# Kernel tuning notes

Measured on AMD Instinct MI355X. Metric: run time of the kernel, lower is better.

## Reference

```python
import jax, jax.numpy as jnp
import numpy as np

N, C, H, W = 32, 2, 512, 512


def setup_inputs() -> dict:
    key = jax.random.key(0)
    k1, k2, k3, k4 = jax.random.split(key, 4)
    inputs = jax.random.uniform(k1, (N, C, H, W), dtype=jnp.float32)
    targets = jax.random.randint(k2, (N, H, W), 0, C, dtype=jnp.int64)
    classes_weights = jax.random.uniform(k3, (C,), dtype=jnp.float32)
    tiles_weights = jax.random.uniform(k4, (N,), dtype=jnp.float32)
    return {"inputs": inputs, "targets": targets,
            "classes_weights": classes_weights, "tiles_weights": tiles_weights,
            "config": 0}


def reference(inputs, targets, classes_weights, tiles_weights, config):
    n, c, h, w = inputs.shape
    p = h * w
    # [C, N, P] layout: vectorize the original's nested class/sample loops
    x = jnp.transpose(inputs.reshape(n, c, p), (1, 0, 2))
    masks = (targets.reshape(n, p)[None] == jnp.arange(c)[:, None, None]).astype(inputs.dtype)
    distance = jnp.abs(masks - x)
    order = jnp.argsort(-distance, axis=-1)  # descending sort per (class, sample)
    d_sorted = jnp.take_along_axis(distance, order, axis=-1)
    m_sorted = jnp.take_along_axis(masks, order, axis=-1)
    gts = jnp.sum(m_sorted, axis=-1, keepdims=True)
    inter = gts - jnp.cumsum(m_sorted, axis=-1)
    union = gts + jnp.cumsum(1.0 - m_sorted, axis=-1)
    iou = 1.0 - inter / union
    # Lovasz gradient: first element kept, then first differences
    grad = jnp.concatenate([iou[..., :1], iou[..., 1:] - iou[..., :-1]], axis=-1)
    per = jnp.sum(d_sorted * grad, axis=-1)  # [C, N]
    # skip condition from original: empty mask AND no prediction above 0.25
    empty = (jnp.sum(masks, axis=-1) == 0) & (jnp.sum(x > 0.25, axis=-1) == 0)
    valid = (classes_weights != 0.0)[:, None] & (~empty)
    weighted = per * tiles_weights[None, :] * classes_weights[:, None]
    loss = jnp.sum(jnp.where(valid, weighted, 0.0))
    non_empty = jnp.sum(valid).astype(inputs.dtype)
    return loss / n / non_empty
```

## Files before the change

kernel.cpp:

```cpp
#include <hip/hip_runtime.h>
#include <hip/hip_bf16.h>
#include <hip/hip_cooperative_groups.h>


#define NB    2048
#define NSEG  64
#define PLOG  18
#define NN    32
#define PTOT  (1 << PLOG)
#define CHUNK (NB / 256)
#define B0_LO (NB / 4)
#define B1_HI (3 * NB / 4)

namespace cg = cooperative_groups;


__device__ __forceinline__ void hist_body(
    const float* __restrict__ x, const int* __restrict__ tgt,
    unsigned* __restrict__ partial, int Bn, int g, unsigned* hl)
{
    const int n = g / Bn, sl = g - n * Bn;
    const int tid = threadIdx.x;
    for (int i = tid; i < 2 * NB; i += 256) hl[i] = 0;
    __syncthreads();

    const int pairs = PTOT / Bn;
    const int base  = sl * pairs;
    const float* x0 = x + (((long long)n * 2) << PLOG);
    const float* x1 = x0 + PTOT;
    const int*   tg = tgt + ((long long)n << PLOG);

    for (int off = tid * 4; off < pairs; off += 256 * 4) {
        const int p = base + off;
        float4 a  = *(const float4*)(x0 + p);
        float4 b  = *(const float4*)(x1 + p);
        int4   t4 = *(const int4*)(tg + p);
        float xa[4] = {a.x, a.y, a.z, a.w};
        float xb[4] = {b.x, b.y, b.z, b.w};
        int   tt[4] = {t4.x, t4.y, t4.z, t4.w};
#pragma unroll
        for (int k = 0; k < 4; ++k) {
            const bool m0 = (tt[k] == 0);
            const bool m1 = (tt[k] == 1);
            float d0 = m0 ? 1.0f - xa[k] : xa[k];
            float d1 = m1 ? 1.0f - xb[k] : xb[k];
            int b0 = min((int)(d0 * (float)NB), NB - 1);
            int b1 = min((int)(d1 * (float)NB), NB - 1);
            atomicAdd(&hl[b0],      m0 ? 0x10000u : 1u);
            atomicAdd(&hl[NB + b1], m1 ? 0x10000u : 1u);
        }
    }
    __syncthreads();
    unsigned* outp = partial + (size_t)g * (2 * NB);
    for (int i = tid; i < 2 * NB; i += 256) outp[i] = hl[i];
}

__device__ __forceinline__ void merge_body(unsigned* __restrict__ partial,
                                           int Bn, int mb)
{
    const int parts = NB / 256;
    const int seg  = mb / parts;
    const int part = mb - seg * parts;
    const int c = seg >> 5, n = seg & 31;
    const int b = part * 256 + threadIdx.x;

    unsigned v0 = 0, v1 = 0;
    for (int s = 0; s < Bn; ++s) {
        unsigned v = partial[(((size_t)(n * Bn + s) * 2) + c) * NB + b];
        v0 += v & 0xFFFFu; v1 += v >> 16;
    }
    partial[(((size_t)(n * Bn + 0) * 2) + c) * NB + b] = v0;
    partial[(((size_t)(n * Bn + 1) * 2) + c) * NB + b] = v1;
}

__device__ __forceinline__ void scan_body(
    const unsigned* __restrict__ partial,
    const float* __restrict__ cw, const float* __restrict__ tw,
    float* __restrict__ segval, unsigned* __restrict__ segvalid,
    int Bn, int seg, unsigned* mh, unsigned* red)
{
    const int c = seg >> 5, n = seg & 31;
    const int tid = threadIdx.x;

    const unsigned* p0 = partial + (((size_t)(n * Bn + 0) * 2) + c) * NB;
    const unsigned* p1 = partial + (((size_t)(n * Bn + 1) * 2) + c) * NB;
    for (int i = tid; i < NB; i += 256) { mh[i] = p0[i]; mh[NB + i] = p1[i]; }
    __syncthreads();

    unsigned tot_all = 0, tot1 = 0, cgt = 0;
    int maxb_local = -1;
    for (int j = 0; j < CHUNK; ++j) {
        int b = (NB - 1) - (tid * CHUNK + j);
        unsigned n0 = mh[b], n1 = mh[NB + b];
        tot_all += n0 + n1; tot1 += n1;
        if (b >= B0_LO) cgt += n0;
        if (b <  B1_HI) cgt += n1;
        if (maxb_local < 0 && (n0 | n1)) maxb_local = b;
    }
    unsigned* sa = red;
    unsigned* s1 = red + 256;
    unsigned* sc = red + 512;
    sa[tid] = tot_all; s1[tid] = tot1; sc[tid] = cgt;
    __syncthreads();
    for (int off = 1; off < 256; off <<= 1) {
        unsigned va = 0, v1 = 0, vc = 0;
        if (tid >= off) { va = sa[tid - off]; v1 = s1[tid - off]; vc = sc[tid - off]; }
        __syncthreads();
        sa[tid] += va; s1[tid] += v1; sc[tid] += vc;
        __syncthreads();
    }
    const unsigned gts   = s1[255];
    const unsigned cntgt = sc[255];
    const unsigned i0  = (tid > 0) ? sa[tid - 1] : 0;
    const unsigned sc0 = (tid > 0) ? s1[tid - 1] : 0;
    __syncthreads();
    ((int*)sc)[tid] = maxb_local;
    __syncthreads();
    for (int off = 128; off > 0; off >>= 1) {
        if (tid < off) ((int*)sc)[tid] = max(((int*)sc)[tid], ((int*)sc)[tid + off]);
        __syncthreads();
    }
    const int max_b = ((int*)sc)[0];

    float per_local = 0.0f;
    if (gts > 0) {
        unsigned i = i0, s = sc0;
        for (int j = 0; j < CHUNK; ++j) {
            int b = (NB - 1) - (tid * CHUNK + j);
            unsigned n0 = mh[b], n1 = mh[NB + b];
            if (n0 | n1) {
                float d_rep = ((float)b + 0.5f) * (1.0f / (float)NB);
                float U = (float)(gts + i - s);
                if (n1) per_local += (float)n1 * d_rep / U;
                s += n1;
                unsigned inter = gts - s;
                if (n0 && inter)
                    per_local += d_rep * (float)inter * (float)n0 /
                                 (U * (U + (float)n0));
                i += n0 + n1;
            }
        }
    }
    __syncthreads();
    float* sd = (float*)sa;
    sd[tid] = per_local;
    __syncthreads();
    for (int off = 128; off > 0; off >>= 1) {
        if (tid < off) sd[tid] += sd[tid + off];
        __syncthreads();
    }
    if (tid == 0) {
        float per = sd[0];
        if (gts == 0)
            per = (max_b >= 0) ? ((float)max_b + 0.5f) * (1.0f / (float)NB) : 0.0f;
        const bool empty = (gts == 0) && (cntgt == 0);
        const float cwv = cw[c], twv = tw[n];
        const bool valid = (cwv != 0.0f) && !empty;
        segval[seg]   = valid ? per * twv * cwv : 0.0f;
        segvalid[seg] = valid ? 1u : 0u;
    }
}

__device__ __forceinline__ void final_body(const float* __restrict__ segval,
                                           const unsigned* __restrict__ segvalid,
                                           float* __restrict__ out)
{
    const int tid = threadIdx.x;
    if (tid < 64) {
        float    lv = segval[tid];
        unsigned vv = segvalid[tid];
        for (int off = 32; off > 0; off >>= 1) {
            lv += __shfl_down(lv, off);
            vv += __shfl_down(vv, off);
        }
        if (tid == 0) out[0] = lv / (float)NN / (float)vv;
    }
}

__global__ __launch_bounds__(256, 8) void lovasz_fused_kernel(
    const float* __restrict__ x, const int* __restrict__ tgt,
    unsigned* __restrict__ partial, float* __restrict__ segval,
    unsigned* __restrict__ segvalid, const float* __restrict__ cw,
    const float* __restrict__ tw, float* __restrict__ out)
{
    __shared__ unsigned hl[2 * NB];
    __shared__ unsigned red[768];
    cg::grid_group grid = cg::this_grid();

    hist_body(x, tgt, partial, 64, blockIdx.x, hl);
    grid.sync();
    if (blockIdx.x < NSEG * (NB / 256))
        merge_body(partial, 64, blockIdx.x);
    grid.sync();
    if (blockIdx.x < NSEG)
        scan_body(partial, cw, tw, segval, segvalid, 64, blockIdx.x, hl, red);
    grid.sync();
    if (blockIdx.x == 0)
        final_body(segval, segvalid, out);
}

__global__ __launch_bounds__(256, 8) void hist_k(
    const float* __restrict__ x, const int* __restrict__ tgt,
    unsigned* __restrict__ partial, int Bn)
{
    __shared__ unsigned hl[2 * NB];
    hist_body(x, tgt, partial, Bn, blockIdx.x, hl);
}

__global__ __launch_bounds__(256) void merge_k(unsigned* __restrict__ partial, int Bn)
{
    merge_body(partial, Bn, blockIdx.x);
}

__global__ __launch_bounds__(256) void scan_k(
    const unsigned* __restrict__ partial, const float* __restrict__ cw,
    const float* __restrict__ tw, float* __restrict__ segval,
    unsigned* __restrict__ segvalid, int Bn)
{
    __shared__ unsigned mh[2 * NB];
    __shared__ unsigned red[768];
    scan_body(partial, cw, tw, segval, segvalid, Bn, blockIdx.x, mh, red);
}

__global__ void final_k(const float* __restrict__ segval,
                        const unsigned* __restrict__ segvalid,
                        float* __restrict__ out)
{
    final_body(segval, segvalid, out);
}

extern "C" void kernel_launch(void* const* d_in, const int* in_sizes, int n_in,
                              void* d_out, int out_size, void* d_ws, size_t ws_size,
                              hipStream_t stream)
{
    const float* x   = (const float*)d_in[0];
    const int*   tgt = (const int*)d_in[1];
    const float* cw  = (const float*)d_in[2];
    const float* tw  = (const float*)d_in[3];
    float* out = (float*)d_out;

    float*    segval   = (float*)d_ws;
    unsigned* segvalid = (unsigned*)((char*)d_ws + 256);
    unsigned* partial  = (unsigned*)((char*)d_ws + 512);

    const size_t per_bn = (size_t)NN * 2 * NB * sizeof(unsigned);
    int Bn = 0;
    if      (ws_size >= 512 + 64 * per_bn) Bn = 64;
    else if (ws_size >= 512 + 32 * per_bn) Bn = 32;
    else                                   Bn = 16;

    bool coop = false;
    if (Bn == 64) {
        int occ = 0, ncu = 0;
        if (hipOccupancyMaxActiveBlocksPerMultiprocessor(
                &occ, lovasz_fused_kernel, 256, 0) == hipSuccess) {
            hipDeviceProp_t prop;
            int dev = 0;
            hipGetDevice(&dev);
            if (hipGetDeviceProperties(&prop, dev) == hipSuccess)
                ncu = prop.multiProcessorCount;
            coop = ((long long)occ * ncu >= (long long)NN * 64);
        }
    }

    if (coop) {
        void* args[] = {(void*)&x, (void*)&tgt, (void*)&partial, (void*)&segval,
                        (void*)&segvalid, (void*)&cw, (void*)&tw, (void*)&out};
        hipLaunchCooperativeKernel((void*)lovasz_fused_kernel,
                                   dim3(NN * 64), dim3(256), args, 0, stream);
    } else {
        hist_k <<<NN * Bn, 256, 0, stream>>>(x, tgt, partial, Bn);
        merge_k<<<NSEG * (NB / 256), 256, 0, stream>>>(partial, Bn);
        scan_k <<<NSEG, 256, 0, stream>>>(partial, cw, tw, segval, segvalid, Bn);
        final_k<<<1, 64, 0, stream>>>(segval, segvalid, out);
    }
}
```

Before: 150.0 us.

## Replace cooperative grid-sync kernel with two launches and atomic final reduction

Drops the cooperative fused kernel and its three grid-wide barriers. The work now runs as two ordinary launches: a histogram kernel, then a merge+scan kernel with 1024-thread blocks that sums partial histograms straight into shared memory. The final reduction moves into the scan kernel through atomics and a last-block-done counter. This removes grid syncs and the separate merge and final passes, but the merge now runs on only 64 blocks, each reading 64 partial histograms, which may underuse the GPU.

```diff
diff --git a/kernel.cpp b/kernel.cpp
--- a/kernel.cpp
+++ b/kernel.cpp
@@ -1,6 +1,5 @@
 #include <hip/hip_runtime.h>
 #include <hip/hip_bf16.h>
-#include <hip/hip_cooperative_groups.h>
 
 
 #define NB    2048
@@ -8,19 +7,27 @@
 #define PLOG  18
 #define NN    32
 #define PTOT  (1 << PLOG)
-#define CHUNK (NB / 256)
 #define B0_LO (NB / 4)
 #define B1_HI (3 * NB / 4)
-
-namespace cg = cooperative_groups;
+#define ST    1024
+#define SCH   (NB / ST)
 
 
-__device__ __forceinline__ void hist_body(
+__global__ __launch_bounds__(256, 8) void hist_k(
     const float* __restrict__ x, const int* __restrict__ tgt,
-    unsigned* __restrict__ partial, int Bn, int g, unsigned* hl)
+    unsigned* __restrict__ partial, float* __restrict__ loss_sum,
+    unsigned* __restrict__ valid_cnt, unsigned* __restrict__ done, int Bn)
 {
-    const int n = g / Bn, sl = g - n * Bn;
+    __shared__ unsigned hl[2 * NB];
+    const int g   = blockIdx.x;
+    const int n   = g / Bn;
+    const int sl  = g - n * Bn;
     const int tid = threadIdx.x;
+
+    if (g == 0 && tid == 0) {
+        *loss_sum = 0.0f; *valid_cnt = 0u; *done = 0u;
+    }
+
     for (int i = tid; i < 2 * NB; i += 256) hl[i] = 0;
     __syncthreads();
 
@@ -55,68 +62,56 @@
     for (int i = tid; i < 2 * NB; i += 256) outp[i] = hl[i];
 }
 
-__device__ __forceinline__ void merge_body(unsigned* __restrict__ partial,
-                                           int Bn, int mb)
+__global__ __launch_bounds__(ST) void mergescan_k(
+    const unsigned* __restrict__ partial, const float* __restrict__ cw,
+    const float* __restrict__ tw, float* __restrict__ loss_sum,
+    unsigned* __restrict__ valid_cnt, unsigned* __restrict__ done,
+    float* __restrict__ out, int Bn)
 {
-    const int parts = NB / 256;
-    const int seg  = mb / parts;
-    const int part = mb - seg * parts;
-    const int c = seg >> 5, n = seg & 31;
-    const int b = part * 256 + threadIdx.x;
-
-    unsigned v0 = 0, v1 = 0;
-    for (int s = 0; s < Bn; ++s) {
-        unsigned v = partial[(((size_t)(n * Bn + s) * 2) + c) * NB + b];
-        v0 += v & 0xFFFFu; v1 += v >> 16;
-    }
-    partial[(((size_t)(n * Bn + 0) * 2) + c) * NB + b] = v0;
-    partial[(((size_t)(n * Bn + 1) * 2) + c) * NB + b] = v1;
-}
-
-__device__ __forceinline__ void scan_body(
-    const unsigned* __restrict__ partial,
-    const float* __restrict__ cw, const float* __restrict__ tw,
-    float* __restrict__ segval, unsigned* __restrict__ segvalid,
-    int Bn, int seg, unsigned* mh, unsigned* red)
-{
+    const int seg = blockIdx.x;
     const int c = seg >> 5, n = seg & 31;
     const int tid = threadIdx.x;
 
-    const unsigned* p0 = partial + (((size_t)(n * Bn + 0) * 2) + c) * NB;
-    const unsigned* p1 = partial + (((size_t)(n * Bn + 1) * 2) + c) * NB;
-    for (int i = tid; i < NB; i += 256) { mh[i] = p0[i]; mh[NB + i] = p1[i]; }
+    __shared__ unsigned mh0[NB], mh1[NB];
+    __shared__ unsigned sa[ST], s1[ST], sc[ST];
+
+    for (int b = tid; b < NB; b += ST) {
+        unsigned v0 = 0, v1 = 0;
+        for (int s = 0; s < Bn; ++s) {
+            unsigned v = partial[(((size_t)(n * Bn + s) * 2) + c) * NB + b];
+            v0 += v & 0xFFFFu; v1 += v >> 16;
+        }
+        mh0[b] = v0; mh1[b] = v1;
+    }
     __syncthreads();
 
     unsigned tot_all = 0, tot1 = 0, cgt = 0;
     int maxb_local = -1;
-    for (int j = 0; j < CHUNK; ++j) {
-        int b = (NB - 1) - (tid * CHUNK + j);
-        unsigned n0 = mh[b], n1 = mh[NB + b];
+    for (int j = 0; j < SCH; ++j) {
+        int b = (NB - 1) - (tid * SCH + j);
+        unsigned n0 = mh0[b], n1 = mh1[b];
         tot_all += n0 + n1; tot1 += n1;
         if (b >= B0_LO) cgt += n0;
         if (b <  B1_HI) cgt += n1;
         if (maxb_local < 0 && (n0 | n1)) maxb_local = b;
     }
-    unsigned* sa = red;
-    unsigned* s1 = red + 256;
-    unsigned* sc = red + 512;
     sa[tid] = tot_all; s1[tid] = tot1; sc[tid] = cgt;
     __syncthreads();
-    for (int off = 1; off < 256; off <<= 1) {
+    for (int off = 1; off < ST; off <<= 1) {
         unsigned va = 0, v1 = 0, vc = 0;
         if (tid >= off) { va = sa[tid - off]; v1 = s1[tid - off]; vc = sc[tid - off]; }
         __syncthreads();
         sa[tid] += va; s1[tid] += v1; sc[tid] += vc;
         __syncthreads();
     }
-    const unsigned gts   = s1[255];
-    const unsigned cntgt = sc[255];
+    const unsigned gts   = s1[ST - 1];
+    const unsigned cntgt = sc[ST - 1];
     const unsigned i0  = (tid > 0) ? sa[tid - 1] : 0;
     const unsigned sc0 = (tid > 0) ? s1[tid - 1] : 0;
     __syncthreads();
     ((int*)sc)[tid] = maxb_local;
     __syncthreads();
-    for (int off = 128; off > 0; off >>= 1) {
+    for (int off = ST / 2; off > 0; off >>= 1) {
         if (tid < off) ((int*)sc)[tid] = max(((int*)sc)[tid], ((int*)sc)[tid + off]);
         __syncthreads();
     }
@@ -125,9 +120,9 @@
     float per_local = 0.0f;
     if (gts > 0) {
         unsigned i = i0, s = sc0;
-        for (int j = 0; j < CHUNK; ++j) {
-            int b = (NB - 1) - (tid * CHUNK + j);
-            unsigned n0 = mh[b], n1 = mh[NB + b];
+        for (int j = 0; j < SCH; ++j) {
+            int b = (NB - 1) - (tid * SCH + j);
+            unsigned n0 = mh0[b], n1 = mh1[b];
             if (n0 | n1) {
                 float d_rep = ((float)b + 0.5f) * (1.0f / (float)NB);
                 float U = (float)(gts + i - s);
@@ -145,10 +140,11 @@
     float* sd = (float*)sa;
     sd[tid] = per_local;
     __syncthreads();
-    for (int off = 128; off > 0; off >>= 1) {
+    for (int off = ST / 2; off > 0; off >>= 1) {
         if (tid < off) sd[tid] += sd[tid + off];
         __syncthreads();
     }
+
     if (tid == 0) {
         float per = sd[0];
         if (gts == 0)
@@ -156,77 +152,18 @@
         const bool empty = (gts == 0) && (cntgt == 0);
         const float cwv = cw[c], twv = tw[n];
         const bool valid = (cwv != 0.0f) && !empty;
-        segval[seg]   = valid ? per * twv * cwv : 0.0f;
-        segvalid[seg] = valid ? 1u : 0u;
+        if (valid) {
+            atomicAdd(loss_sum, per * twv * cwv);
+            atomicAdd(valid_cnt, 1u);
+        }
+        __threadfence();
+        unsigned old = atomicAdd(done, 1u);
+        if (old == NSEG - 1) {
+            float    L = atomicAdd(loss_sum, 0.0f);
+            unsigned V = atomicAdd(valid_cnt, 0u);
+            out[0] = L / (float)NN / (float)V;
+        }
     }
-}
-
-__device__ __forceinline__ void final_body(const float* __restrict__ segval,
-                                           const unsigned* __restrict__ segvalid,
-                                           float* __restrict__ out)
-{
-    const int tid = threadIdx.x;
-    if (tid < 64) {
-        float    lv = segval[tid];
-        unsigned vv = segvalid[tid];
-        for (int off = 32; off > 0; off >>= 1) {
-            lv += __shfl_down(lv, off);
-            vv += __shfl_down(vv, off);
-        }
-        if (tid == 0) out[0] = lv / (float)NN / (float)vv;
-    }
-}
-
-__global__ __launch_bounds__(256, 8) void lovasz_fused_kernel(
-    const float* __restrict__ x, const int* __restrict__ tgt,
-    unsigned* __restrict__ partial, float* __restrict__ segval,
-    unsigned* __restrict__ segvalid, const float* __restrict__ cw,
-    const float* __restrict__ tw, float* __restrict__ out)
-{
-    __shared__ unsigned hl[2 * NB];
-    __shared__ unsigned red[768];
-    cg::grid_group grid = cg::this_grid();
-
-    hist_body(x, tgt, partial, 64, blockIdx.x, hl);
-    grid.sync();
-    if (blockIdx.x < NSEG * (NB / 256))
-        merge_body(partial, 64, blockIdx.x);
-    grid.sync();
-    if (blockIdx.x < NSEG)
-        scan_body(partial, cw, tw, segval, segvalid, 64, blockIdx.x, hl, red);
-    grid.sync();
-    if (blockIdx.x == 0)
-        final_body(segval, segvalid, out);
-}
-
-__global__ __launch_bounds__(256, 8) void hist_k(
-    const float* __restrict__ x, const int* __restrict__ tgt,
-    unsigned* __restrict__ partial, int Bn)
-{
-    __shared__ unsigned hl[2 * NB];
-    hist_body(x, tgt, partial, Bn, blockIdx.x, hl);
-}
-
-__global__ __launch_bounds__(256) void merge_k(unsigned* __restrict__ partial, int Bn)
-{
-    merge_body(partial, Bn, blockIdx.x);
-}
-
-__global__ __launch_bounds__(256) void scan_k(
-    const unsigned* __restrict__ partial, const float* __restrict__ cw,
-    const float* __restrict__ tw, float* __restrict__ segval,
-    unsigned* __restrict__ segvalid, int Bn)
-{
-    __shared__ unsigned mh[2 * NB];
-    __shared__ unsigned red[768];
-    scan_body(partial, cw, tw, segval, segvalid, Bn, blockIdx.x, mh, red);
-}
-
-__global__ void final_k(const float* __restrict__ segval,
-                        const unsigned* __restrict__ segvalid,
-                        float* __restrict__ out)
-{
-    final_body(segval, segvalid, out);
 }
 
 extern "C" void kernel_launch(void* const* d_in, const int* in_sizes, int n_in,
@@ -239,39 +176,19 @@
     const float* tw  = (const float*)d_in[3];
     float* out = (float*)d_out;
 
-    float*    segval   = (float*)d_ws;
-    unsigned* segvalid = (unsigned*)((char*)d_ws + 256);
-    unsigned* partial  = (unsigned*)((char*)d_ws + 512);
+    float*    loss_sum  = (float*)d_ws;
+    unsigned* valid_cnt = (unsigned*)((char*)d_ws + 4);
+    unsigned* done      = (unsigned*)((char*)d_ws + 8);
+    unsigned* partial   = (unsigned*)((char*)d_ws + 512);
 
     const size_t per_bn = (size_t)NN * 2 * NB * sizeof(unsigned);
-    int Bn = 0;
+    int Bn;
     if      (ws_size >= 512 + 64 * per_bn) Bn = 64;
     else if (ws_size >= 512 + 32 * per_bn) Bn = 32;
     else                                   Bn = 16;
 
-    bool coop = false;
-    if (Bn == 64) {
-        int occ = 0, ncu = 0;
-        if (hipOccupancyMaxActiveBlocksPerMultiprocessor(
-                &occ, lovasz_fused_kernel, 256, 0) == hipSuccess) {
-            hipDeviceProp_t prop;
-            int dev = 0;
-            hipGetDevice(&dev);
-            if (hipGetDeviceProperties(&prop, dev) == hipSuccess)
-                ncu = prop.multiProcessorCount;
-            coop = ((long long)occ * ncu >= (long long)NN * 64);
-        }
-    }
-
-    if (coop) {
-        void* args[] = {(void*)&x, (void*)&tgt, (void*)&partial, (void*)&segval,
-                        (void*)&segvalid, (void*)&cw, (void*)&tw, (void*)&out};
-        hipLaunchCooperativeKernel((void*)lovasz_fused_kernel,
-                                   dim3(NN * 64), dim3(256), args, 0, stream);
-    } else {
-        hist_k <<<NN * Bn, 256, 0, stream>>>(x, tgt, partial, Bn);
-        merge_k<<<NSEG * (NB / 256), 256, 0, stream>>>(partial, Bn);
-        scan_k <<<NSEG, 256, 0, stream>>>(partial, cw, tw, segval, segvalid, Bn);
-        final_k<<<1, 64, 0, stream>>>(segval, segvalid, out);
-    }
+    hist_k     <<<NN * Bn, 256, 0, stream>>>(x, tgt, partial, loss_sum,
+                                             valid_cnt, done, Bn);
+    mergescan_k<<<NSEG, ST, 0, stream>>>(partial, cw, tw, loss_sum,
+                                         valid_cnt, done, out, Bn);
 }
```

Measured after the change: 156.6 us. 4.4% more time.
